# Kernel optimization log

Hardware: AMD Instinct MI355X
Metric: run time of the kernel (lower is better)

## Reference

```python
import jax, jax.numpy as jnp
import numpy as np

D, DFFN, H, P, L = 256, 1024, 8, 4, 4
B, LQ = 32, 300
LENS = [2048, 1024, 512, 256]
STARTS = [0, 2048, 3072, 3584]
S = sum(LENS)


def setup_inputs() -> dict:
    key = jax.random.key(0)
    ks = iter(jax.random.split(key, 64))
    def W(shape, s=0.02):
        return jax.random.normal(next(ks), shape, jnp.float32) * s
    inp = {}
    inp['tgt'] = W((B, LQ, D), 1.0)
    inp['query_pos'] = W((B, LQ, D), 1.0)
    centers = jax.random.uniform(next(ks), (B, LQ, L))
    widths = 0.05 + 0.2 * jax.random.uniform(next(ks), (B, LQ, L))
    inp['reference_points'] = jnp.stack([centers, widths], -1)  # (B,Lq,L,2) = (center,width)
    inp['src'] = W((B, S, D), 1.0)
    inp['temporal_lengths'] = np.array(LENS, np.int64)
    inp['level_start_index'] = np.array(STARTS, np.int64)
    for n, shape in [('sa_qw', (D, D)), ('sa_kw', (D, D)), ('sa_vw', (D, D)), ('sa_ow', (D, D)), ('ff1_w', (D, DFFN)), ('ff2_w', (DFFN, D))]:
        inp[n] = W(shape)
    for n, sz in [('sa_qb', D), ('sa_kb', D), ('sa_vb', D), ('sa_ob', D), ('ff1_b', DFFN), ('ff2_b', D)]:
        inp[n] = jnp.zeros((sz,), jnp.float32)
    for pre in ['ca', 'se']:
        inp[pre + '_off_w'] = W((D, H * L * P))
        inp[pre + '_off_b'] = jnp.zeros((H * L * P,), jnp.float32)
        inp[pre + '_attn_w'] = W((D, H * L * P))
        inp[pre + '_attn_b'] = jnp.zeros((H * L * P,), jnp.float32)
        inp[pre + '_val_w'] = W((D, D))
        inp[pre + '_val_b'] = jnp.zeros((D,), jnp.float32)
        inp[pre + '_out_w'] = W((D, D))
        inp[pre + '_out_b'] = jnp.zeros((D,), jnp.float32)
    for n in ['ln1', 'lnse', 'ln2', 'ln3']:
        inp[n + '_g'] = jnp.ones((D,), jnp.float32)
        inp[n + '_b'] = jnp.zeros((D,), jnp.float32)
    return inp


def _ln(x, g, b, eps=1e-5):
    m = jnp.mean(x, -1, keepdims=True)
    v = jnp.mean((x - m) ** 2, -1, keepdims=True)
    return (x - m) * jax.lax.rsqrt(v + eps) * g + b


def _mha(q, k, v, qw, qb, kw, kb, vw, vb, ow, ob):
    b, lq, d = q.shape
    dh = d // H
    qh = (q @ qw + qb).reshape(b, lq, H, dh).transpose(0, 2, 1, 3)
    kh = (k @ kw + kb).reshape(b, -1, H, dh).transpose(0, 2, 1, 3)
    vh = (v @ vw + vb).reshape(b, -1, H, dh).transpose(0, 2, 1, 3)
    scores = jnp.einsum('bhqd,bhkd->bhqk', qh, kh) * (dh ** -0.5)
    attn = jax.nn.softmax(scores, -1)
    out = jnp.einsum('bhqk,bhkd->bhqd', attn, vh).transpose(0, 2, 1, 3).reshape(b, lq, d)
    return out @ ow + ob


def _deform(q, ref, src, lens, starts, vw, vb, offw, offb, aw, ab, ow, ob, boundary):
    b, lq, d = q.shape
    dh = d // H
    value = (src @ vw + vb).reshape(b, -1, H, dh)  # (B,S,H,Dh)
    off = (q @ offw + offb).reshape(b, lq, H, L, P)
    attn = jax.nn.softmax((q @ aw + ab).reshape(b, lq, H, L * P), -1).reshape(b, lq, H, L, P)
    center = ref[..., 0][:, :, None, :, None]  # (B,Lq,1,L,1)
    width = ref[..., 1][:, :, None, :, None]
    if boundary:
        # half the points anchored at segment start, half at segment end
        sign = jnp.where(jnp.arange(P) < P // 2, -0.5, 0.5)
        anchor = center + sign * width
    else:
        anchor = center
    loc = anchor + off / P * width * 0.5  # normalized sampling locations (B,Lq,H,L,P)
    out = jnp.zeros((b, lq, H, dh), value.dtype)
    for l in range(L):
        T = int(lens[l]); s0 = int(starts[l])
        v = value[:, s0:s0 + T].transpose(0, 2, 1, 3)  # (B,H,T,Dh)
        x = loc[:, :, :, l, :] * T - 0.5  # align_corners=False grid
        x0 = jnp.floor(x)
        w = x - x0
        i0 = x0.astype(jnp.int32)
        i1 = i0 + 1
        m0 = ((i0 >= 0) & (i0 < T)).astype(v.dtype)
        m1 = ((i1 >= 0) & (i1 < T)).astype(v.dtype)
        i0c = jnp.clip(i0, 0, T - 1)
        i1c = jnp.clip(i1, 0, T - 1)
        def gather(idx):
            idxh = idx.transpose(0, 2, 1, 3).reshape(b, H, lq * P, 1)
            g = jnp.take_along_axis(v, jnp.broadcast_to(idxh, (b, H, lq * P, dh)), axis=2)
            return g.reshape(b, H, lq, P, dh).transpose(0, 2, 1, 3, 4)  # (B,Lq,H,P,Dh)
        samp = gather(i0c) * ((1 - w) * m0)[..., None] + gather(i1c) * (w * m1)[..., None]
        out = out + jnp.einsum('bqhp,bqhpd->bqhd', attn[:, :, :, l, :], samp)
    return out.reshape(b, lq, d) @ ow + ob


def reference(tgt, query_pos, reference_points, src, temporal_lengths, level_start_index,
              sa_qw, sa_qb, sa_kw, sa_kb, sa_vw, sa_vb, sa_ow, sa_ob,
              ca_off_w, ca_off_b, ca_attn_w, ca_attn_b, ca_val_w, ca_val_b, ca_out_w, ca_out_b,
              se_off_w, se_off_b, se_attn_w, se_attn_b, se_val_w, se_val_b, se_out_w, se_out_b,
              ff1_w, ff1_b, ff2_w, ff2_b,
              ln1_g, ln1_b, lnse_g, lnse_b, ln2_g, ln2_b, ln3_g, ln3_b):
    lens = np.asarray(temporal_lengths)
    starts = np.asarray(level_start_index)
    q = tgt + query_pos
    t2 = _mha(q, q, tgt, sa_qw, sa_qb, sa_kw, sa_kb, sa_vw, sa_vb, sa_ow, sa_ob)
    tgt = _ln(tgt + t2, ln2_g, ln2_b)
    t2 = _deform(tgt + query_pos, reference_points, src, lens, starts,
                 ca_val_w, ca_val_b, ca_off_w, ca_off_b, ca_attn_w, ca_attn_b, ca_out_w, ca_out_b, False)
    tgt = _ln(tgt + t2, ln1_g, ln1_b)
    t2 = _deform(tgt + query_pos, reference_points, src, lens, starts,
                 se_val_w, se_val_b, se_off_w, se_off_b, se_attn_w, se_attn_b, se_out_w, se_out_b, True)
    tgt = _ln(tgt + t2, lnse_g, lnse_b)
    t2 = jax.nn.relu(tgt @ ff1_w + ff1_b) @ ff2_w + ff2_b
    tgt = _ln(tgt + t2, ln3_g, ln3_b)
    return tgt
```

## Files before the change

kernel.cpp:

```cpp
#include <hip/hip_runtime.h>
#include <hip/hip_bf16.h>

namespace {

typedef unsigned short u16;
typedef unsigned int u32;

constexpr int D    = 256;
constexpr int H    = 8;
constexpr int DH   = 32;
constexpr int B    = 32;
constexpr int LQ   = 300;
constexpr int NQ   = B * LQ;
constexpr int S    = 3840;
constexpr int MS   = B * S;
constexpr int DFFN = 1024;

typedef __attribute__((ext_vector_type(8))) short bf16x8;
typedef __attribute__((ext_vector_type(4))) float f32x4;

__device__ inline u16 f2b(float x) {
  u32 u = __builtin_bit_cast(u32, x);
  u32 r = (u + 0x7FFFu + ((u >> 16) & 1u)) >> 16;
  return (u16)r;
}
__device__ inline u32 pk2(float a, float b) {
  return (u32)f2b(a) | ((u32)f2b(b) << 16);
}
__device__ inline void unpack2(u32 w, float& a, float& b) {
  a = __builtin_bit_cast(float, w << 16);
  b = __builtin_bit_cast(float, w & 0xffff0000u);
}

template<bool OUT_BF16, bool RELU>
__global__ __launch_bounds__(256) void gemm_sm(
    const u16* __restrict__ A, const u16* __restrict__ Bt,
    const float* __restrict__ bias, void* __restrict__ Cv,
    int M, int K, int N)
{
  constexpr int BM = 64, BN = 64, BK = 64, LDK = 72;
  __shared__ __align__(16) u16 sh[(BM + BN) * LDK];
  u16* As = sh;
  u16* Bs = sh + BM * LDK;
  const int tid  = threadIdx.x;
  const int lane = tid & 63;
  const int wid  = tid >> 6;
  const int wm = wid >> 1, wn = wid & 1;
  const int m0 = blockIdx.y * BM, n0 = blockIdx.x * BN;

  f32x4 acc[2][2] = {};
  uint4 ra[2], rb[2];
  const int NT = K / BK;
  const int srow = tid >> 3, sch = (tid & 7) * 8;

#pragma unroll
  for (int i = 0; i < 2; ++i) {
    const int row = srow + i * 32;
    ra[i] = *(const uint4*)(A  + (size_t)(m0 + row) * K + sch);
    rb[i] = *(const uint4*)(Bt + (size_t)(n0 + row) * K + sch);
  }

  for (int t = 0; t < NT; ++t) {
#pragma unroll
    for (int i = 0; i < 2; ++i) {
      const int row = srow + i * 32;
      *(uint4*)(&As[row * LDK + sch]) = ra[i];
      *(uint4*)(&Bs[row * LDK + sch]) = rb[i];
    }
    __syncthreads();
    if (t + 1 < NT) {
      const int k0 = (t + 1) * BK;
#pragma unroll
      for (int i = 0; i < 2; ++i) {
        const int row = srow + i * 32;
        ra[i] = *(const uint4*)(A  + (size_t)(m0 + row) * K + k0 + sch);
        rb[i] = *(const uint4*)(Bt + (size_t)(n0 + row) * K + k0 + sch);
      }
    }
#pragma unroll
    for (int kk = 0; kk < 2; ++kk) {
      const int krd = kk * 32 + (lane >> 4) * 8;
      bf16x8 af[2], bf[2];
#pragma unroll
      for (int m = 0; m < 2; ++m)
        af[m] = *(const bf16x8*)(&As[(wm * 32 + (lane & 15) + 16 * m) * LDK + krd]);
#pragma unroll
      for (int n = 0; n < 2; ++n)
        bf[n] = *(const bf16x8*)(&Bs[(wn * 32 + (lane & 15) + 16 * n) * LDK + krd]);
#pragma unroll
      for (int m = 0; m < 2; ++m)
#pragma unroll
        for (int n = 0; n < 2; ++n)
          acc[m][n] = __builtin_amdgcn_mfma_f32_16x16x32_bf16(af[m], bf[n], acc[m][n], 0, 0, 0);
    }
    __syncthreads();
  }

  const int cr = (lane >> 4) * 4;
  const int cc = lane & 15;
  if constexpr (OUT_BF16) {
    u16* stg = sh;
#pragma unroll
    for (int n = 0; n < 2; ++n) {
      const int lc = wn * 32 + n * 16 + cc;
      const float bv = bias[n0 + lc];
#pragma unroll
      for (int m = 0; m < 2; ++m) {
        const int lr0 = wm * 32 + m * 16 + cr;
#pragma unroll
        for (int r = 0; r < 4; ++r) {
          float x = acc[m][n][r] + bv;
          if (RELU) x = fmaxf(x, 0.f);
          stg[(lr0 + r) * LDK + lc] = f2b(x);
        }
      }
    }
    __syncthreads();
    u16* Cb = (u16*)Cv;
#pragma unroll
    for (int i = 0; i < 2; ++i) {
      const int c = tid + 256 * i;
      const int row = c >> 3, ch = c & 7;
      *(uint4*)(Cb + (size_t)(m0 + row) * N + n0 + ch * 8) =
          *(const uint4*)(&stg[row * LDK + ch * 8]);
    }
  } else {
#pragma unroll
    for (int n = 0; n < 2; ++n) {
      const int gc = n0 + wn * 32 + n * 16 + cc;
      const float bv = bias[gc];
#pragma unroll
      for (int m = 0; m < 2; ++m) {
        const int gr0 = m0 + wm * 32 + m * 16 + cr;
#pragma unroll
        for (int r = 0; r < 4; ++r) {
          float x = acc[m][n][r] + bv;
          if (RELU) x = fmaxf(x, 0.f);
          ((float*)Cv)[(size_t)(gr0 + r) * N + gc] = x;
        }
      }
    }
  }
}

__global__ __launch_bounds__(256) void gemm_qkv(
    const u16* __restrict__ qbuf, const u16* __restrict__ tgtb,
    const u16* __restrict__ saqk_t, const u16* __restrict__ sav_t,
    const float* __restrict__ qkb, const float* __restrict__ vbias,
    u16* __restrict__ qkbuf, u16* __restrict__ vh)
{
  constexpr int K = 256, BK = 64, LDK = 72;
  __shared__ __align__(16) u16 sh[128 * LDK];
  u16* As = sh;
  u16* Bs = sh + 64 * LDK;
  const bool isv = blockIdx.x >= 8;
  const u16* A  = isv ? tgtb : qbuf;
  const u16* Bt = isv ? sav_t : saqk_t;
  const float* bias = isv ? vbias : qkb;
  u16* C = isv ? vh : qkbuf;
  const int N = isv ? 256 : 512;
  const int n0 = (isv ? (int)blockIdx.x - 8 : (int)blockIdx.x) * 64;
  const int m0 = blockIdx.y * 64;

  const int tid  = threadIdx.x;
  const int lane = tid & 63;
  const int wid  = tid >> 6;
  const int wm = wid >> 1, wn = wid & 1;

  f32x4 acc[2][2] = {};
  uint4 ra[2], rb[2];
  const int srow = tid >> 3, sch = (tid & 7) * 8;

#pragma unroll
  for (int i = 0; i < 2; ++i) {
    const int row = srow + i * 32;
    ra[i] = *(const uint4*)(A  + (size_t)(m0 + row) * K + sch);
    rb[i] = *(const uint4*)(Bt + (size_t)(n0 + row) * K + sch);
  }
  for (int t = 0; t < 4; ++t) {
#pragma unroll
    for (int i = 0; i < 2; ++i) {
      const int row = srow + i * 32;
      *(uint4*)(&As[row * LDK + sch]) = ra[i];
      *(uint4*)(&Bs[row * LDK + sch]) = rb[i];
    }
    __syncthreads();
    if (t + 1 < 4) {
      const int k0 = (t + 1) * BK;
#pragma unroll
      for (int i = 0; i < 2; ++i) {
        const int row = srow + i * 32;
        ra[i] = *(const uint4*)(A  + (size_t)(m0 + row) * K + k0 + sch);
        rb[i] = *(const uint4*)(Bt + (size_t)(n0 + row) * K + k0 + sch);
      }
    }
#pragma unroll
    for (int kk = 0; kk < 2; ++kk) {
      const int krd = kk * 32 + (lane >> 4) * 8;
      bf16x8 af[2], bf[2];
#pragma unroll
      for (int m = 0; m < 2; ++m)
        af[m] = *(const bf16x8*)(&As[(wm * 32 + (lane & 15) + 16 * m) * LDK + krd]);
#pragma unroll
      for (int n = 0; n < 2; ++n)
        bf[n] = *(const bf16x8*)(&Bs[(wn * 32 + (lane & 15) + 16 * n) * LDK + krd]);
#pragma unroll
      for (int m = 0; m < 2; ++m)
#pragma unroll
        for (int n = 0; n < 2; ++n)
          acc[m][n] = __builtin_amdgcn_mfma_f32_16x16x32_bf16(af[m], bf[n], acc[m][n], 0, 0, 0);
    }
    __syncthreads();
  }

  const int cr = (lane >> 4) * 4;
  const int cc = lane & 15;
  u16* stg = sh;
#pragma unroll
  for (int n = 0; n < 2; ++n) {
    const int lc = wn * 32 + n * 16 + cc;
    const float bv = bias[n0 + lc];
#pragma unroll
    for (int m = 0; m < 2; ++m) {
      const int lr0 = wm * 32 + m * 16 + cr;
#pragma unroll
      for (int r = 0; r < 4; ++r)
        stg[(lr0 + r) * LDK + lc] = f2b(acc[m][n][r] + bv);
    }
  }
  __syncthreads();
#pragma unroll
  for (int i = 0; i < 2; ++i) {
    const int c = tid + 256 * i;
    const int row = c >> 3, ch = c & 7;
    *(uint4*)(C + (size_t)(m0 + row) * N + n0 + ch * 8) =
        *(const uint4*)(&stg[row * LDK + ch * 8]);
  }
}

__global__ __launch_bounds__(512) void gemm_val4(
    const float* __restrict__ A, const u16* __restrict__ Bt2,
    const float* __restrict__ bias2, u16* __restrict__ Vca, u16* __restrict__ Vse)
{
  __shared__ __align__(16) char shraw[33792];
  char* Asw = shraw;
  const int tid  = threadIdx.x;
  const int lane = tid & 63;
  const int w    = tid >> 6;
  const int nh   = blockIdx.x & 1;
  const int m0   = (blockIdx.x >> 1) * 64;
  u16* dst = nh ? Vse : Vca;
  const u16* Bt = Bt2 + nh * 256 * 256;
  const float* bias = bias2 + nh * 256;
  const int b  = m0 / S;
  const int s0 = m0 - b * S;

#pragma unroll
  for (int i = 0; i < 4; ++i) {
    const int idx = tid + 512 * i;
    const int row = idx >> 5, ch = idx & 31;
    const float* ap = A + (size_t)(m0 + row) * 256 + ch * 8;
    const float4 f0 = *(const float4*)(ap);
    const float4 f1 = *(const float4*)(ap + 4);
    uint4 pk;
    pk.x = pk2(f0.x, f0.y); pk.y = pk2(f0.z, f0.w);
    pk.z = pk2(f1.x, f1.y); pk.w = pk2(f1.z, f1.w);
    *(uint4*)(Asw + row * 512 + ((ch * 16) ^ ((row & 7) << 4))) = pk;
  }
  __syncthreads();

  f32x4 acc[4][2] = {};
  const u16* bb = Bt + (size_t)(w * 32 + (lane & 15)) * 256 + (lane >> 4) * 8;
  bf16x8 bcur[2], bnxt[2];
#pragma unroll
  for (int n = 0; n < 2; ++n) bcur[n] = *(const bf16x8*)(bb + n * 4096);

#pragma unroll
  for (int kk = 0; kk < 8; ++kk) {
    bf16x8 af[4];
    const int kb = kk * 64 + (lane >> 4) * 16;
#pragma unroll
    for (int m = 0; m < 4; ++m) {
      const int row = m * 16 + (lane & 15);
      af[m] = *(const bf16x8*)(Asw + row * 512 + (kb ^ ((row & 7) << 4)));
    }
    if (kk < 7) {
#pragma unroll
      for (int n = 0; n < 2; ++n)
        bnxt[n] = *(const bf16x8*)(bb + n * 4096 + (kk + 1) * 32);
    }
#pragma unroll
    for (int m = 0; m < 4; ++m)
#pragma unroll
      for (int n = 0; n < 2; ++n)
        acc[m][n] = __builtin_amdgcn_mfma_f32_16x16x32_bf16(af[m], bcur[n], acc[m][n], 0, 0, 0);
#pragma unroll
    for (int n = 0; n < 2; ++n) bcur[n] = bnxt[n];
  }
  __syncthreads();

  constexpr int STC = 264;
  u16* stg = (u16*)shraw;
  const int cr = (lane >> 4) * 4;
  const int cc = lane & 15;
#pragma unroll
  for (int n = 0; n < 2; ++n) {
    const int col = w * 32 + n * 16 + cc;
    const float bv = bias[col];
#pragma unroll
    for (int m = 0; m < 4; ++m) {
      const int r0 = m * 16 + cr;
#pragma unroll
      for (int r = 0; r < 4; ++r)
        stg[(r0 + r) * STC + col] = f2b(acc[m][n][r] + bv);
    }
  }
  __syncthreads();
  u16* vb = dst + (size_t)b * H * S * DH;
#pragma unroll
  for (int i = 0; i < 4; ++i) {
    const int c = tid + 512 * i;
    const int row = c >> 5, ch = c & 31;
    const int h = ch >> 2, dq = ch & 3;
    *(uint4*)(vb + ((size_t)h * S + (s0 + row)) * DH + dq * 8) =
        *(const uint4*)(&stg[row * STC + ch * 8]);
  }
}

template<int MODE>
__global__ __launch_bounds__(1024) void gemm_ln(
    const u16* __restrict__ A, const u16* __restrict__ Bt,
    const float* __restrict__ bias, const float* __restrict__ res,
    const float* __restrict__ g, const float* __restrict__ be,
    const float* __restrict__ qpos,
    float* __restrict__ fout, u16* __restrict__ bfout, int K)
{
  constexpr int BK = 64, LDK = 72;
  __shared__ __align__(16) float ftile[64 * 264];
  u16* As = (u16*)ftile;
  u16* Bs = As + 64 * LDK;
  const int tid  = threadIdx.x;
  const int lane = tid & 63;
  const int wid  = tid >> 6;
  const int wm = wid >> 2, wn = wid & 3;
  const int m0 = blockIdx.x * 64;

  f32x4 acc[4] = {};
  const int NT = K / BK;
  const bool am = tid < 512;
  const int arow = tid >> 3, ach = (tid & 7) * 8;

  uint4 ra = {};
  uint4 rb[2];
  if (am) ra = *(const uint4*)(A + (size_t)(m0 + arow) * K + ach);
#pragma unroll
  for (int i = 0; i < 2; ++i) {
    const int idx = tid + 1024 * i;
    const int brow = idx >> 3, bch = (idx & 7) * 8;
    rb[i] = *(const uint4*)(Bt + (size_t)brow * K + bch);
  }

  for (int t = 0; t < NT; ++t) {
    if (am) *(uint4*)(&As[arow * LDK + ach]) = ra;
#pragma unroll
    for (int i = 0; i < 2; ++i) {
      const int idx = tid + 1024 * i;
      const int brow = idx >> 3, bch = (idx & 7) * 8;
      *(uint4*)(&Bs[brow * LDK + bch]) = rb[i];
    }
    __syncthreads();
    if (t + 1 < NT) {
      const int k0 = (t + 1) * BK;
      if (am) ra = *(const uint4*)(A + (size_t)(m0 + arow) * K + k0 + ach);
#pragma unroll
      for (int i = 0; i < 2; ++i) {
        const int idx = tid + 1024 * i;
        const int brow = idx >> 3, bch = (idx & 7) * 8;
        rb[i] = *(const uint4*)(Bt + (size_t)brow * K + k0 + bch);
      }
    }
#pragma unroll
    for (int kk = 0; kk < 2; ++kk) {
      const int krd = kk * 32 + (lane >> 4) * 8;
      bf16x8 af, bf[4];
      af = *(const bf16x8*)(&As[(wm * 16 + (lane & 15)) * LDK + krd]);
#pragma unroll
      for (int n = 0; n < 4; ++n)
        bf[n] = *(const bf16x8*)(&Bs[(wn * 64 + n * 16 + (lane & 15)) * LDK + krd]);
#pragma unroll
      for (int n = 0; n < 4; ++n)
        acc[n] = __builtin_amdgcn_mfma_f32_16x16x32_bf16(af, bf[n], acc[n], 0, 0, 0);
    }
    __syncthreads();
  }

  const int cr = (lane >> 4) * 4;
  const int cc = lane & 15;
#pragma unroll
  for (int n = 0; n < 4; ++n) {
    const int col = wn * 64 + n * 16 + cc;
    const float bv = bias[col];
#pragma unroll
    for (int r = 0; r < 4; ++r)
      ftile[(wm * 16 + cr + r) * 264 + col] = acc[n][r] + bv;
  }
  __syncthreads();

  const int row = tid >> 4, s16 = tid & 15;
  const size_t grow = (size_t)(m0 + row) * 256;
  float vv[16];
  float sum = 0.f;
#pragma unroll
  for (int j = 0; j < 4; ++j) {
    const int col = s16 * 4 + j * 64;
    const float4 fv = *(const float4*)(&ftile[row * 264 + col]);
    const float4 rv = *(const float4*)(res + grow + col);
    vv[j * 4 + 0] = fv.x + rv.x; vv[j * 4 + 1] = fv.y + rv.y;
    vv[j * 4 + 2] = fv.z + rv.z; vv[j * 4 + 3] = fv.w + rv.w;
    sum += vv[j * 4 + 0] + vv[j * 4 + 1] + vv[j * 4 + 2] + vv[j * 4 + 3];
  }
  sum += __shfl_xor(sum, 1, 64);
  sum += __shfl_xor(sum, 2, 64);
  sum += __shfl_xor(sum, 4, 64);
  sum += __shfl_xor(sum, 8, 64);
  const float mean = sum * (1.f / 256.f);
  float sq = 0.f;
#pragma unroll
  for (int k = 0; k < 16; ++k) { const float d = vv[k] - mean; sq += d * d; }
  sq += __shfl_xor(sq, 1, 64);
  sq += __shfl_xor(sq, 2, 64);
  sq += __shfl_xor(sq, 4, 64);
  sq += __shfl_xor(sq, 8, 64);
  const float rstd = rsqrtf(sq * (1.f / 256.f) + 1e-5f);

#pragma unroll
  for (int j = 0; j < 4; ++j) {
    const int col = s16 * 4 + j * 64;
    const float4 gv = *(const float4*)(g + col);
    const float4 bv = *(const float4*)(be + col);
    float4 y;
    y.x = (vv[j * 4 + 0] - mean) * rstd * gv.x + bv.x;
    y.y = (vv[j * 4 + 1] - mean) * rstd * gv.y + bv.y;
    y.z = (vv[j * 4 + 2] - mean) * rstd * gv.z + bv.z;
    y.w = (vv[j * 4 + 3] - mean) * rstd * gv.w + bv.w;
    *(float4*)(fout + grow + col) = y;
    if constexpr (MODE == 0) {
      const float4 qv = *(const float4*)(qpos + grow + col);
      uint2 pk;
      pk.x = pk2(y.x + qv.x, y.y + qv.y);
      pk.y = pk2(y.z + qv.z, y.w + qv.w);
      *(uint2*)(bfout + grow + col) = pk;
    } else if constexpr (MODE == 1) {
      uint2 pk;
      pk.x = pk2(y.x, y.y);
      pk.y = pk2(y.z, y.w);
      *(uint2*)(bfout + grow + col) = pk;
    }
  }
}

struct WSpec { const float* w; u16* wt; int K, N, blk0; };
struct WPack { WSpec s[14]; };

struct PrepArgs {
  const float *ca_off_b, *ca_attn_b, *se_off_b, *se_attn_b;
  const float *sa_qb, *sa_kb, *ca_val_b, *se_val_b;
  float *bias4, *qkb, *valb;
  const float *tgt, *qpos;
  u16 *tgtb, *qbuf;
  int n4, nwt;
};

__global__ __launch_bounds__(256) void prep_all(WPack p, PrepArgs a) {
  __shared__ float tile[32][33];
  const int b = blockIdx.x;
  if (b < a.nwt) {
    int i = 0;
#pragma unroll
    for (int j = 1; j < 14; ++j) if (b >= p.s[j].blk0) i = j;
    const float* w = p.s[i].w;
    u16* wt = p.s[i].wt;
    const int K = p.s[i].K, N = p.s[i].N;
    const int lb = b - p.s[i].blk0;
    const int ntN = N >> 5;
    const int tk = lb / ntN, tn = lb - tk * ntN;
    const int r = threadIdx.x >> 5, c = threadIdx.x & 31;
#pragma unroll
    for (int j = 0; j < 4; ++j)
      tile[r + j * 8][c] = w[(size_t)(tk * 32 + r + j * 8) * N + tn * 32 + c];
    __syncthreads();
#pragma unroll
    for (int j = 0; j < 4; ++j)
      wt[(size_t)(tn * 32 + r + j * 8) * K + tk * 32 + c] = f2b(tile[c][r + j * 8]);
  } else if (b == a.nwt) {
#pragma unroll
    for (int u = 0; u < 2; ++u) {
      const int t = threadIdx.x + 256 * u;
      a.bias4[t] = t < 128 ? a.ca_off_b[t] : t < 256 ? a.ca_attn_b[t - 128]
                 : t < 384 ? a.se_off_b[t - 256] : a.se_attn_b[t - 384];
      a.qkb[t]  = t < 256 ? a.sa_qb[t] : a.sa_kb[t - 256];
      a.valb[t] = t < 256 ? a.ca_val_b[t] : a.se_val_b[t - 256];
    }
  } else {
    const int i = (b - a.nwt - 1) * 256 + threadIdx.x;
    if (i < a.n4) {
      const float4 t = ((const float4*)a.tgt)[i];
      const float4 q = ((const float4*)a.qpos)[i];
      uint2 x, y;
      x.x = pk2(t.x, t.y); x.y = pk2(t.z, t.w);
      y.x = pk2(t.x + q.x, t.y + q.y); y.y = pk2(t.z + q.z, t.w + q.w);
      ((uint2*)a.tgtb)[i] = x;
      ((uint2*)a.qbuf)[i] = y;
    }
  }
}

__global__ __launch_bounds__(512) void mha_v2(
    const u16* __restrict__ qk, const u16* __restrict__ vh,
    u16* __restrict__ out)
{
  __shared__ __align__(16) float Ks[8 * 300 * 4];
  __shared__ __align__(16) float Vs[8 * 300 * 4];
  const int bh  = blockIdx.x & 255;
  const int seg = blockIdx.x >> 8;
  const int b = bh >> 3, h = bh & 7;
  const u16* kbase = qk + (size_t)b * LQ * 512 + 256 + h * DH;
  const u16* vbase = vh + (size_t)b * LQ * D + h * DH;
  for (int e = threadIdx.x; e < 300 * 8; e += 512) {
    const int r = e >> 3, j = e & 7;
    float4 f;
    const uint2 kv = *(const uint2*)(kbase + (size_t)r * 512 + j * 4);
    unpack2(kv.x, f.x, f.y);
    unpack2(kv.y, f.z, f.w);
    *(float4*)(&Ks[(j * 300 + r) * 4]) = f;
    const uint2 vv = *(const uint2*)(vbase + (size_t)r * D + j * 4);
    unpack2(vv.x, f.x, f.y);
    unpack2(vv.y, f.z, f.w);
    *(float4*)(&Vs[(j * 300 + r) * 4]) = f;
  }
  __syncthreads();

  const int lane = threadIdx.x & 63;
  const int lq = (threadIdx.x >> 6) * 16 + (lane >> 2);
  const int kc = lane & 3;
  const int q = seg * 128 + lq;
  if (q >= LQ) return;

  const u16* qrow = qk + (size_t)(b * LQ + q) * 512 + h * DH;
  float qv[DH];
#pragma unroll
  for (int c4 = 0; c4 < 4; ++c4) {
    const uint4 u = *(const uint4*)(qrow + c4 * 8);
    unpack2(u.x, qv[c4 * 8 + 0], qv[c4 * 8 + 1]);
    unpack2(u.y, qv[c4 * 8 + 2], qv[c4 * 8 + 3]);
    unpack2(u.z, qv[c4 * 8 + 4], qv[c4 * 8 + 5]);
    unpack2(u.w, qv[c4 * 8 + 6], qv[c4 * 8 + 7]);
  }
#pragma unroll
  for (int d = 0; d < DH; ++d) qv[d] *= 0.17677669529663689f;

  float o[DH] = {};
  float ssum = 0.f;
  const float* kp = &Ks[kc * 75 * 4];
  const float* vp = &Vs[kc * 75 * 4];
  for (int i = 0; i < 75; ++i) {
    float s = 0.f;
#pragma unroll
    for (int j = 0; j < 8; ++j) {
      const float4 kf = *(const float4*)(kp + i * 4 + j * 1200);
      s += qv[j * 4 + 0] * kf.x + qv[j * 4 + 1] * kf.y
         + qv[j * 4 + 2] * kf.z + qv[j * 4 + 3] * kf.w;
    }
    const float p = __expf(s);
    ssum += p;
#pragma unroll
    for (int j = 0; j < 8; ++j) {
      const float4 vf = *(const float4*)(vp + i * 4 + j * 1200);
      o[j * 4 + 0] += p * vf.x; o[j * 4 + 1] += p * vf.y;
      o[j * 4 + 2] += p * vf.z; o[j * 4 + 3] += p * vf.w;
    }
  }

  ssum += __shfl_xor(ssum, 1, 64);
  ssum += __shfl_xor(ssum, 2, 64);
#pragma unroll
  for (int d = 0; d < DH; ++d) {
    o[d] += __shfl_xor(o[d], 1, 64);
    o[d] += __shfl_xor(o[d], 2, 64);
  }
  const float inv = 1.f / ssum;

  u16* orow = out + (size_t)(b * LQ + q) * D + h * DH;
#pragma unroll
  for (int c = 0; c < 4; ++c) {
    if (kc == c) {
      uint4 w;
      w.x = pk2(o[c * 8 + 0] * inv, o[c * 8 + 1] * inv);
      w.y = pk2(o[c * 8 + 2] * inv, o[c * 8 + 3] * inv);
      w.z = pk2(o[c * 8 + 4] * inv, o[c * 8 + 5] * inv);
      w.w = pk2(o[c * 8 + 6] * inv, o[c * 8 + 7] * inv);
      *(uint4*)(orow + c * 8) = w;
    }
  }
}

template<bool BOUNDARY>
__global__ __launch_bounds__(512) void deform_v4(
    const float* __restrict__ oa, const float* __restrict__ ref,
    const u16* __restrict__ value, u16* __restrict__ out)
{
  __shared__ __align__(16) uint4 owt[4][128];
  const int unit = threadIdx.x >> 7;
  const int bq = blockIdx.x * 4 + unit;
  const int b = bq / LQ;
  const int t = threadIdx.x & 127;
  const int h = t >> 4;
  const int l = (t >> 2) & 3;
  const int p = t & 3;

  const float off   = oa[(size_t)bq * 256 + t];
  const float logit = oa[(size_t)bq * 256 + 128 + t];
  const float center = ref[(size_t)bq * 8 + l * 2 + 0];
  const float width  = ref[(size_t)bq * 8 + l * 2 + 1];

  const float e = __expf(logit);
  float ssum = e;
  ssum += __shfl_xor(ssum, 1, 64);
  ssum += __shfl_xor(ssum, 2, 64);
  ssum += __shfl_xor(ssum, 4, 64);
  ssum += __shfl_xor(ssum, 8, 64);
  const float wa = e / ssum;

  const int T  = 2048 >> l;
  const int s0 = 4096 - (4096 >> l);
  float anchor = center;
  if (BOUNDARY) anchor += (p < 2 ? -0.5f : 0.5f) * width;
  const float loc = anchor + off * width * 0.125f;
  const float x = loc * (float)T - 0.5f;
  const float x0 = floorf(x);
  const float w = x - x0;
  const int i0 = (int)x0;
  const int i1 = i0 + 1;
  const float w0 = (i0 >= 0 && i0 < T) ? wa * (1.f - w) : 0.f;
  const float w1 = (i1 >= 0 && i1 < T) ? wa * w : 0.f;
  const int i0c = min(max(i0, 0), T - 1);
  const int i1c = min(max(i1, 0), T - 1);
  uint4 pack;
  pack.x = (u32)((h * S + s0 + i0c) * (DH * 2));
  pack.y = __builtin_bit_cast(u32, w0);
  pack.z = (u32)((h * S + s0 + i1c) * (DH * 2));
  pack.w = __builtin_bit_cast(u32, w1);
  owt[unit][t] = pack;
  __syncthreads();

  const int g  = t >> 4;
  const int ln = t & 15;
  const int qd = ln & 3;
  const int ts = ln >> 2;
  const char* vb = (const char*)(value + (size_t)b * H * S * DH) + qd * 16;
  float o[8] = {};
#pragma unroll
  for (int i = 0; i < 8; ++i) {
    const int rowidx = i * 4 + ts;
    const uint4 ow = owt[unit][g * 16 + (rowidx >> 1)];
    const u32 boff = (rowidx & 1) ? ow.z : ow.x;
    const float wt = __builtin_bit_cast(float, (rowidx & 1) ? ow.w : ow.y);
    const uint4 v = *(const uint4*)(vb + boff);
    float a0, a1;
    unpack2(v.x, a0, a1); o[0] += wt * a0; o[1] += wt * a1;
    unpack2(v.y, a0, a1); o[2] += wt * a0; o[3] += wt * a1;
    unpack2(v.z, a0, a1); o[4] += wt * a0; o[5] += wt * a1;
    unpack2(v.w, a0, a1); o[6] += wt * a0; o[7] += wt * a1;
  }
#pragma unroll
  for (int d = 0; d < 8; ++d) {
    o[d] += __shfl_xor(o[d], 4, 64);
    o[d] += __shfl_xor(o[d], 8, 64);
  }
  if (ts == 0) {
    uint4 wv;
    wv.x = pk2(o[0], o[1]); wv.y = pk2(o[2], o[3]);
    wv.z = pk2(o[4], o[5]); wv.w = pk2(o[6], o[7]);
    *(uint4*)(out + (size_t)bq * D + g * DH + qd * 8) = wv;
  }
}

}

extern "C" void kernel_launch(void* const* d_in, const int* in_sizes, int n_in,
                              void* d_out, int out_size, void* d_ws, size_t ws_size,
                              hipStream_t stream)
{
  const float* tgt   = (const float*)d_in[0];
  const float* qpos  = (const float*)d_in[1];
  const float* ref   = (const float*)d_in[2];
  const float* src   = (const float*)d_in[3];
  const float* sa_qw = (const float*)d_in[6];
  const float* sa_kw = (const float*)d_in[7];
  const float* sa_vw = (const float*)d_in[8];
  const float* sa_ow = (const float*)d_in[9];
  const float* ff1_w = (const float*)d_in[10];
  const float* ff2_w = (const float*)d_in[11];
  const float* sa_qb = (const float*)d_in[12];
  const float* sa_kb = (const float*)d_in[13];
  const float* sa_vb = (const float*)d_in[14];
  const float* sa_ob = (const float*)d_in[15];
  const float* ff1_b = (const float*)d_in[16];
  const float* ff2_b = (const float*)d_in[17];
  const float* ca_off_w  = (const float*)d_in[18];
  const float* ca_off_b  = (const float*)d_in[19];
  const float* ca_attn_w = (const float*)d_in[20];
  const float* ca_attn_b = (const float*)d_in[21];
  const float* ca_val_w  = (const float*)d_in[22];
  const float* ca_val_b  = (const float*)d_in[23];
  const float* ca_out_w  = (const float*)d_in[24];
  const float* ca_out_b  = (const float*)d_in[25];
  const float* se_off_w  = (const float*)d_in[26];
  const float* se_off_b  = (const float*)d_in[27];
  const float* se_attn_w = (const float*)d_in[28];
  const float* se_attn_b = (const float*)d_in[29];
  const float* se_val_w  = (const float*)d_in[30];
  const float* se_val_b  = (const float*)d_in[31];
  const float* se_out_w  = (const float*)d_in[32];
  const float* se_out_b  = (const float*)d_in[33];
  const float* ln1_g  = (const float*)d_in[34];
  const float* ln1_b  = (const float*)d_in[35];
  const float* lnse_g = (const float*)d_in[36];
  const float* lnse_b = (const float*)d_in[37];
  const float* ln2_g  = (const float*)d_in[38];
  const float* ln2_b  = (const float*)d_in[39];
  const float* ln3_g  = (const float*)d_in[40];
  const float* ln3_b  = (const float*)d_in[41];

  const size_t ND = (size_t)NQ * D;
  const size_t MD = (size_t)MS * D;

  char* base = (char*)d_ws;
  size_t off = 0;
  auto alloc = [&](size_t bytes) -> void* {
    void* p = base + off;
    off += (bytes + 255) & ~(size_t)255;
    return p;
  };
  u16*  Vca  = (u16*)alloc(MD * 2);
  u16*  Vse  = (u16*)alloc(MD * 2);
  u16*  qkbuf = (u16*)alloc((size_t)NQ * 512 * 2);
  u16*  vh   = (u16*)alloc(ND * 2);
  u16*  qbuf = (u16*)alloc(ND * 2);
  u16*  smpb = (u16*)alloc(ND * 2);
  u16*  tgtb = (u16*)alloc(ND * 2);
  u16*  curb = (u16*)alloc(ND * 2);
  float* cur = (float*)alloc(ND * 4);
  float* oabuf = (float*)alloc((size_t)NQ * 256 * 4);
  float* bias4 = (float*)alloc(512 * 4);
  float* qkb   = (float*)alloc(512 * 4);
  float* valb  = (float*)alloc(512 * 4);

  u16* ffh = Vca;

  WPack pk;
  int wi = 0, blk = 0;
  auto addw = [&](const float* w, int K, int N) -> u16* {
    u16* wt = (u16*)alloc((size_t)K * N * 2);
    pk.s[wi].w = w; pk.s[wi].wt = wt; pk.s[wi].K = K; pk.s[wi].N = N; pk.s[wi].blk0 = blk;
    blk += (K / 32) * (N / 32);
    ++wi;
    return wt;
  };
  u16* saq_t = addw(sa_qw, D, D);
  u16* sak_t = addw(sa_kw, D, D);        (void)sak_t;
  u16* sav_t = addw(sa_vw, D, D);
  u16* sao_t = addw(sa_ow, D, D);
  u16* ff1_t = addw(ff1_w, D, DFFN);
  u16* ff2_t = addw(ff2_w, DFFN, D);
  u16* caoff_t = addw(ca_off_w, D, 128);
  u16* caatt_t = addw(ca_attn_w, D, 128);  (void)caatt_t;
  u16* seoff_t = addw(se_off_w, D, 128);
  u16* seatt_t = addw(se_attn_w, D, 128);  (void)seatt_t;
  u16* caval_t = addw(ca_val_w, D, D);
  u16* seval_t = addw(se_val_w, D, D);     (void)seval_t;
  u16* caout_t = addw(ca_out_w, D, D);
  u16* seout_t = addw(se_out_w, D, D);

  const int n4 = (int)(ND / 4);

  PrepArgs pa;
  pa.ca_off_b = ca_off_b; pa.ca_attn_b = ca_attn_b;
  pa.se_off_b = se_off_b; pa.se_attn_b = se_attn_b;
  pa.sa_qb = sa_qb; pa.sa_kb = sa_kb; pa.ca_val_b = ca_val_b; pa.se_val_b = se_val_b;
  pa.bias4 = bias4; pa.qkb = qkb; pa.valb = valb;
  pa.tgt = tgt; pa.qpos = qpos; pa.tgtb = tgtb; pa.qbuf = qbuf;
  pa.n4 = n4; pa.nwt = blk;
  prep_all<<<blk + 1 + 2400, 256, 0, stream>>>(pk, pa);

  gemm_val4<<<(MS / 64) * 2, 512, 0, stream>>>(src, caval_t, valb, Vca, Vse);

  gemm_qkv<<<dim3(12, 150), 256, 0, stream>>>(qbuf, tgtb, saq_t, sav_t, qkb, sa_vb, qkbuf, vh);
  mha_v2<<<B * H * 3, 512, 0, stream>>>(qkbuf, vh, smpb);
  gemm_ln<0><<<NQ / 64, 1024, 0, stream>>>(smpb, sao_t, sa_ob, tgt, ln2_g, ln2_b, qpos, cur, qbuf, D);

  gemm_sm<false, false><<<dim3(4, 150), 256, 0, stream>>>(qbuf, caoff_t, bias4, oabuf, NQ, D, 256);
  deform_v4<false><<<NQ / 4, 512, 0, stream>>>(oabuf, ref, Vca, smpb);
  gemm_ln<0><<<NQ / 64, 1024, 0, stream>>>(smpb, caout_t, ca_out_b, cur, ln1_g, ln1_b, qpos, cur, qbuf, D);

  gemm_sm<false, false><<<dim3(4, 150), 256, 0, stream>>>(qbuf, seoff_t, bias4 + 256, oabuf, NQ, D, 256);
  deform_v4<true><<<NQ / 4, 512, 0, stream>>>(oabuf, ref, Vse, smpb);
  gemm_ln<1><<<NQ / 64, 1024, 0, stream>>>(smpb, seout_t, se_out_b, cur, lnse_g, lnse_b, nullptr, cur, curb, D);

  gemm_sm<true,  true ><<<dim3(16, 150), 256, 0, stream>>>(curb, ff1_t, ff1_b, ffh, NQ, D, DFFN);
  gemm_ln<2><<<NQ / 64, 1024, 0, stream>>>(ffh, ff2_t, ff2_b, cur, ln3_g, ln3_b, nullptr, (float*)d_out, nullptr, DFFN);
}
```

Before: 467.2 us.

## Fuse FFN up-projection, ReLU, down-projection and LayerNorm into one kernel

Replaces the separate FF1 GEMM and FF2+LayerNorm kernels with one kernel that processes 32-row tiles. Each tile computes the 1024-wide ReLU hidden activation into swizzled LDS as bf16, then runs the second GEMM and the residual LayerNorm in the same block. This removes the global-memory round trip of the NQ x 1024 hidden tensor and one launch. In exchange it uses 80KB of LDS per block, which limits occupancy, and every block rereads both weight matrices from global or L2.

```diff
diff --git a/kernel.cpp b/kernel.cpp
--- a/kernel.cpp
+++ b/kernel.cpp
@@ -456,6 +456,150 @@
       pk.y = pk2(y.z, y.w);
       *(uint2*)(bfout + grow + col) = pk;
     }
+  }
+}
+
+__global__ __launch_bounds__(512) void gemm_ffn(
+    const u16* __restrict__ A, const u16* __restrict__ B1t,
+    const u16* __restrict__ B2t, const float* __restrict__ b1,
+    const float* __restrict__ b2, const float* __restrict__ res,
+    const float* __restrict__ g, const float* __restrict__ be,
+    float* __restrict__ fout)
+{
+  __shared__ __align__(16) char sh[81920];
+  char* Ast = sh;
+  char* ffh = sh + 16384;
+  const int tid  = threadIdx.x;
+  const int lane = tid & 63;
+  const int w    = tid >> 6;
+  const int m0   = blockIdx.x * 32;
+
+#pragma unroll
+  for (int i = 0; i < 2; ++i) {
+    const int idx = tid + 512 * i;
+    const int row = idx >> 5, ch = idx & 31;
+    const uint4 v = *(const uint4*)(A + (size_t)(m0 + row) * 256 + ch * 8);
+    *(uint4*)(Ast + row * 512 + ((ch * 16) ^ ((row & 7) << 4))) = v;
+  }
+  __syncthreads();
+
+  {
+    f32x4 acc[2][8] = {};
+    const u16* bb = B1t + (size_t)(w * 128 + (lane & 15)) * 256 + (lane >> 4) * 8;
+#pragma unroll
+    for (int kk = 0; kk < 8; ++kk) {
+      bf16x8 af[2];
+      const int kb = kk * 64 + (lane >> 4) * 16;
+#pragma unroll
+      for (int m = 0; m < 2; ++m) {
+        const int row = m * 16 + (lane & 15);
+        af[m] = *(const bf16x8*)(Ast + row * 512 + (kb ^ ((row & 7) << 4)));
+      }
+#pragma unroll
+      for (int n = 0; n < 8; ++n) {
+        const bf16x8 bf = *(const bf16x8*)(bb + (size_t)n * 16 * 256 + kk * 32);
+#pragma unroll
+        for (int m = 0; m < 2; ++m)
+          acc[m][n] = __builtin_amdgcn_mfma_f32_16x16x32_bf16(af[m], bf, acc[m][n], 0, 0, 0);
+      }
+    }
+    const int cr = (lane >> 4) * 4;
+    const int cc = lane & 15;
+#pragma unroll
+    for (int n = 0; n < 8; ++n) {
+      const int col = w * 128 + n * 16 + cc;
+      const float bv = b1[col];
+#pragma unroll
+      for (int m = 0; m < 2; ++m) {
+#pragma unroll
+        for (int r = 0; r < 4; ++r) {
+          const int row = m * 16 + cr + r;
+          const float x = fmaxf(acc[m][n][r] + bv, 0.f);
+          *(u16*)(ffh + row * 2048 + ((col * 2) ^ ((row & 7) << 4))) = f2b(x);
+        }
+      }
+    }
+  }
+  __syncthreads();
+
+  f32x4 acc2[2][2] = {};
+  {
+    const u16* bb = B2t + (size_t)(w * 32 + (lane & 15)) * 1024 + (lane >> 4) * 8;
+#pragma unroll 4
+    for (int kk = 0; kk < 32; ++kk) {
+      bf16x8 af[2];
+      const int kb = kk * 64 + (lane >> 4) * 16;
+#pragma unroll
+      for (int m = 0; m < 2; ++m) {
+        const int row = m * 16 + (lane & 15);
+        af[m] = *(const bf16x8*)(ffh + row * 2048 + (kb ^ ((row & 7) << 4)));
+      }
+#pragma unroll
+      for (int n = 0; n < 2; ++n) {
+        const bf16x8 bf = *(const bf16x8*)(bb + (size_t)n * 16 * 1024 + kk * 32);
+#pragma unroll
+        for (int m = 0; m < 2; ++m)
+          acc2[m][n] = __builtin_amdgcn_mfma_f32_16x16x32_bf16(af[m], bf, acc2[m][n], 0, 0, 0);
+      }
+    }
+  }
+  __syncthreads();
+
+  float* ftile = (float*)sh;
+  {
+    const int cr = (lane >> 4) * 4;
+    const int cc = lane & 15;
+#pragma unroll
+    for (int n = 0; n < 2; ++n) {
+      const int col = w * 32 + n * 16 + cc;
+      const float bv = b2[col];
+#pragma unroll
+      for (int m = 0; m < 2; ++m)
+#pragma unroll
+        for (int r = 0; r < 4; ++r)
+          ftile[(m * 16 + cr + r) * 264 + col] = acc2[m][n][r] + bv;
+    }
+  }
+  __syncthreads();
+
+  const int row = tid >> 4, s16 = tid & 15;
+  const size_t grow = (size_t)(m0 + row) * 256;
+  float vv[16];
+  float sum = 0.f;
+#pragma unroll
+  for (int j = 0; j < 4; ++j) {
+    const int col = s16 * 4 + j * 64;
+    const float4 fv = *(const float4*)(&ftile[row * 264 + col]);
+    const float4 rv = *(const float4*)(res + grow + col);
+    vv[j * 4 + 0] = fv.x + rv.x; vv[j * 4 + 1] = fv.y + rv.y;
+    vv[j * 4 + 2] = fv.z + rv.z; vv[j * 4 + 3] = fv.w + rv.w;
+    sum += vv[j * 4 + 0] + vv[j * 4 + 1] + vv[j * 4 + 2] + vv[j * 4 + 3];
+  }
+  sum += __shfl_xor(sum, 1, 64);
+  sum += __shfl_xor(sum, 2, 64);
+  sum += __shfl_xor(sum, 4, 64);
+  sum += __shfl_xor(sum, 8, 64);
+  const float mean = sum * (1.f / 256.f);
+  float sq = 0.f;
+#pragma unroll
+  for (int k = 0; k < 16; ++k) { const float d = vv[k] - mean; sq += d * d; }
+  sq += __shfl_xor(sq, 1, 64);
+  sq += __shfl_xor(sq, 2, 64);
+  sq += __shfl_xor(sq, 4, 64);
+  sq += __shfl_xor(sq, 8, 64);
+  const float rstd = rsqrtf(sq * (1.f / 256.f) + 1e-5f);
+
+#pragma unroll
+  for (int j = 0; j < 4; ++j) {
+    const int col = s16 * 4 + j * 64;
+    const float4 gv = *(const float4*)(g + col);
+    const float4 bv = *(const float4*)(be + col);
+    float4 y;
+    y.x = (vv[j * 4 + 0] - mean) * rstd * gv.x + bv.x;
+    y.y = (vv[j * 4 + 1] - mean) * rstd * gv.y + bv.y;
+    y.z = (vv[j * 4 + 2] - mean) * rstd * gv.z + bv.z;
+    y.w = (vv[j * 4 + 3] - mean) * rstd * gv.w + bv.w;
+    *(float4*)(fout + grow + col) = y;
   }
 }
 
@@ -756,8 +900,6 @@
   float* qkb   = (float*)alloc(512 * 4);
   float* valb  = (float*)alloc(512 * 4);
 
-  u16* ffh = Vca;
-
   WPack pk;
   int wi = 0, blk = 0;
   auto addw = [&](const float* w, int K, int N) -> u16* {
@@ -807,6 +949,6 @@
   deform_v4<true><<<NQ / 4, 512, 0, stream>>>(oabuf, ref, Vse, smpb);
   gemm_ln<1><<<NQ / 64, 1024, 0, stream>>>(smpb, seout_t, se_out_b, cur, lnse_g, lnse_b, nullptr, cur, curb, D);
 
-  gemm_sm<true,  true ><<<dim3(16, 150), 256, 0, stream>>>(curb, ff1_t, ff1_b, ffh, NQ, D, DFFN);
-  gemm_ln<2><<<NQ / 64, 1024, 0, stream>>>(ffh, ff2_t, ff2_b, cur, ln3_g, ln3_b, nullptr, (float*)d_out, nullptr, DFFN);
-}
+  gemm_ffn<<<NQ / 32, 512, 0, stream>>>(curb, ff1_t, ff2_t, ff1_b, ff2_b, cur,
+                                        ln3_g, ln3_b, (float*)d_out);
+}
```

Result: faster. 431.9 us (-7.6%).
